# Performance work log

Hardware: AMD Instinct MI355X
Metric: run time of the kernel (lower is better)

## Reference

```python
import jax, jax.numpy as jnp
import numpy as np

B, T, C = 2, 2048, 2048
H = 16
HS = C // H           # 128
ROT = HS // 2         # 64 partial-rotary dims
BASE = 10000.0


def setup_inputs() -> dict:
    key = jax.random.key(0)
    ks = jax.random.split(key, 9)
    s = 1.0 / np.sqrt(C)
    return {
        "x": jax.random.normal(ks[0], (B, T, C), jnp.float32),
        "Wq": jax.random.normal(ks[1], (C, C), jnp.float32) * s,
        "bq": jax.random.normal(ks[2], (C,), jnp.float32) * 0.02,
        "Wk": jax.random.normal(ks[3], (C, C), jnp.float32) * s,
        "bk": jax.random.normal(ks[4], (C,), jnp.float32) * 0.02,
        "Wv": jax.random.normal(ks[5], (C, C), jnp.float32) * s,
        "bv": jax.random.normal(ks[6], (C,), jnp.float32) * 0.02,
        "Wo": jax.random.normal(ks[7], (C, C), jnp.float32) * s,
        "bo": jax.random.normal(ks[8], (C,), jnp.float32) * 0.02,
    }


def _rotate_half(u):
    u1, u2 = u[..., : u.shape[-1] // 2], u[..., u.shape[-1] // 2 :]
    return jnp.concatenate((-u2, u1), axis=-1)


def _rope_tables(t_len):
    inv_freq = 1.0 / (BASE ** (jnp.arange(0, ROT, 2, dtype=jnp.float32) / ROT))
    freqs = jnp.arange(t_len, dtype=jnp.float32)[:, None] * inv_freq[None, :]
    emb = jnp.concatenate((freqs, freqs), axis=-1)  # [T, ROT]
    return jnp.cos(emb), jnp.sin(emb)


def reference(x, Wq, bq, Wk, bk, Wv, bv, Wo, bo):
    Bs, Ts, Cs = x.shape
    q = (x @ Wq.T + bq).reshape(Bs, Ts, H, HS).transpose(0, 2, 1, 3)  # [B,H,T,HS]
    k = (x @ Wk.T + bk).reshape(Bs, Ts, H, HS).transpose(0, 2, 1, 3)
    v = (x @ Wv.T + bv).reshape(Bs, Ts, H, HS).transpose(0, 2, 1, 3)

    # partial rotary on first ROT dims of each head
    cos, sin = _rope_tables(Ts)  # [T, ROT] broadcast over B,H
    q_rot, q_pass = q[..., :ROT], q[..., ROT:]
    k_rot, k_pass = k[..., :ROT], k[..., ROT:]
    q_rot = q_rot * cos + _rotate_half(q_rot) * sin
    k_rot = k_rot * cos + _rotate_half(k_rot) * sin
    q = jnp.concatenate((q_rot, q_pass), axis=-1)
    k = jnp.concatenate((k_rot, k_pass), axis=-1)

    att = jnp.einsum("bhqd,bhkd->bhqk", q, k) * (1.0 / np.sqrt(HS))
    causal = jnp.tril(jnp.ones((Ts, Ts), dtype=bool))
    att = jnp.where(causal, att, jnp.float32(-jnp.inf))
    att = jax.nn.softmax(att, axis=-1)
    out = jnp.einsum("bhqk,bhkd->bhqd", att, v)          # [B,H,T,HS]
    out = out.transpose(0, 2, 1, 3).reshape(Bs, Ts, Cs)  # [B,T,C]
    return out @ Wo.T + bo
```

## Files before the change

### kernel.cpp

```cpp
#include <hip/hip_runtime.h>
#include <hip/hip_bf16.h>

#define Bdim 2
#define Tdim 2048
#define Cdim 2048
#define Hn   16

using bf16x8 = __attribute__((ext_vector_type(8))) short;
using f32x4  = __attribute__((ext_vector_type(4))) float;
using f32x16 = __attribute__((ext_vector_type(16))) float;
typedef __hip_bfloat16 bf16;

#define VMWAIT(n) asm volatile("s_waitcnt vmcnt(" #n ")" ::: "memory")
#define CROW(r, hi) (((r) & 3) + 8 * ((r) >> 2) + 4 * (hi))
#define QS2 ((float)(0.08838834764831845 * 1.4426950408889634))
#define THR2 11.5415603f

__device__ __forceinline__ void load_lds16(const void* g, void* l) {
  __builtin_amdgcn_global_load_lds(
      (const __attribute__((address_space(1))) void*)g,
      (__attribute__((address_space(3))) void*)l, 16, 0, 0);
}

__device__ __forceinline__ float bf2f(unsigned short u) {
  union { unsigned int i; float f; } x; x.i = ((unsigned int)u) << 16; return x.f;
}
__device__ __forceinline__ unsigned short f2bf(float f) {
  bf16 h = __float2bfloat16(f); return *(unsigned short*)&h;
}
__device__ __forceinline__ unsigned cvtpk(float lo, float hi) {
  unsigned r;
  asm volatile("v_cvt_pk_bf16_f32 %0, %1, %2" : "=v"(r) : "v"(lo), "v"(hi));
  return r;
}

__global__ __launch_bounds__(256) void cvt_all(const float* __restrict__ x,
                                               const float* __restrict__ w0,
                                               const float* __restrict__ w1,
                                               const float* __restrict__ w2,
                                               const float* __restrict__ w3,
                                               bf16* __restrict__ dx,
                                               bf16* __restrict__ d0,
                                               bf16* __restrict__ d1,
                                               bf16* __restrict__ d2,
                                               bf16* __restrict__ d3) {
  const int NX = (Bdim * Tdim * Cdim) / 4;
  const int NW = (Cdim * Cdim) / 4;
  int i = blockIdx.x * 256 + threadIdx.x;
  int stride = gridDim.x * 256;
  for (; i < NX + 4 * NW; i += stride) {
    const float* s; bf16* d; int j;
    if (i < NX) { s = x; d = dx; j = i; }
    else {
      int k = i - NX;
      int wsel = k >> 20;
      j = k & (NW - 1);
      s = wsel == 0 ? w0 : wsel == 1 ? w1 : wsel == 2 ? w2 : w3;
      d = wsel == 0 ? d0 : wsel == 1 ? d1 : wsel == 2 ? d2 : d3;
    }
    float4 v = ((const float4*)s)[j];
    ushort4 o;
    o.x = f2bf(v.x); o.y = f2bf(v.y); o.z = f2bf(v.z); o.w = f2bf(v.w);
    ((ushort4*)d)[j] = o;
  }
}

__global__ __launch_bounds__(256) void rope_tables_k(float2* __restrict__ cst) {
  int idx = blockIdx.x * blockDim.x + threadIdx.x;
  if (idx >= Tdim * 32) return;
  int t = idx >> 5, i = idx & 31;
  double f = pow(10000.0, -(double)i / 32.0);
  double ang = (double)t * f;
  cst[idx] = make_float2((float)cos(ang), (float)sin(ang));
}

__global__ __launch_bounds__(256, 2) void gemmQKV(
    const bf16* __restrict__ A, const bf16* __restrict__ Wcat,
    const float* __restrict__ b0, const float* __restrict__ b1, const float* __restrict__ b2,
    bf16* __restrict__ oq, bf16* __restrict__ ok, bf16* __restrict__ vt,
    const float2* __restrict__ cst) {
  extern __shared__ char lds[];
  const int tid = threadIdx.x, lane = tid & 63, wid = tid >> 6;
  const int l31 = lane & 31, hi = lane >> 5;
  const int wr = wid >> 1, wc = wid & 1;
  const int wbase = wid * 1024;

  const int q8 = gridDim.x >> 3;
  const int swz = ((int)blockIdx.x & 7) * q8 + ((int)blockIdx.x >> 3);
  const int bm = (swz >> 5) * 256;
  const int strip = swz & 31;

  const int rS = tid >> 2, sS = tid & 3;
  const int ssw = (sS ^ ((rS >> 1) & 3)) << 3;
  const bf16* thrA = A + (size_t)(bm + rS) * 2048 + ssw;
  const bf16* thrB = Wcat + (size_t)(strip * 192 + rS) * 2048 + ssw;

#define SA(T, DB) { load_lds16(thrA + (T) * 32, (DB) + wbase);                              \
                    load_lds16(thrA + (size_t)64 * 2048 + (T) * 32, (DB) + 4096 + wbase);   \
                    load_lds16(thrA + (size_t)128 * 2048 + (T) * 32, (DB) + 8192 + wbase);  \
                    load_lds16(thrA + (size_t)192 * 2048 + (T) * 32, (DB) + 12288 + wbase); }
#define SB(T, DB) { load_lds16(thrB + (T) * 32, (DB) + 16384 + wbase);                      \
                    load_lds16(thrB + (size_t)64 * 2048 + (T) * 32, (DB) + 20480 + wbase);  \
                    load_lds16(thrB + (size_t)128 * 2048 + (T) * 32, (DB) + 24576 + wbase); }

  f32x16 acc[4][3] = {};
  bf16x8 afr[4], bfr[3];
  const int q2 = (l31 >> 1) & 3;
  const int aoff = (wr * 128 + l31) * 64;
  const int boff = 16384 + (wc * 96 + l31) * 64;
  const int sl0 = (hi ^ q2) << 4;
  const int sl1 = sl0 ^ 32;

#define READF(PB, SL)                                                        \
  {                                                                          \
    const char* _p = (PB);                                                   \
    _Pragma("unroll")                                                        \
    for (int m_ = 0; m_ < 4; ++m_)                                           \
      afr[m_] = *(const bf16x8*)(_p + aoff + m_ * 2048 + (SL));              \
    _Pragma("unroll")                                                        \
    for (int n_ = 0; n_ < 3; ++n_)                                           \
      bfr[n_] = *(const bf16x8*)(_p + boff + n_ * 2048 + (SL));              \
  }

#define MF12()                                                               \
  __builtin_amdgcn_s_setprio(1);                                             \
  _Pragma("unroll")                                                          \
  for (int m_ = 0; m_ < 4; ++m_)                                             \
    _Pragma("unroll")                                                        \
    for (int n_ = 0; n_ < 3; ++n_)                                           \
      acc[m_][n_] = __builtin_amdgcn_mfma_f32_32x32x16_bf16(                 \
          afr[m_], bfr[n_], acc[m_][n_], 0, 0, 0);                           \
  __builtin_amdgcn_s_setprio(0);

  SA(0, lds); SB(0, lds);
  VMWAIT(0);
  __builtin_amdgcn_s_barrier();
  __builtin_amdgcn_sched_barrier(0);
  READF(lds, sl0);

  const int NT = 64;
  for (int t = 0; t < NT; ++t) {
    char* bufC = lds + (t & 1) * 28672;
    char* bufO = lds + ((t + 1) & 1) * 28672;
    if (t + 1 < NT) { SA(t + 1, bufO); SB(t + 1, bufO); }
    MF12();
    READF(bufC, sl1);
    MF12();
    if (t + 1 < NT) {
      VMWAIT(0);
      __builtin_amdgcn_s_barrier();
      __builtin_amdgcn_sched_barrier(0);
      READF(bufO, sl0);
    }
  }

  __syncthreads();
  if (wc == 1 && (strip & 1)) {
    const int col0 = strip * 192 + 96;
    const int mat = col0 >> 11;
    if (mat < 2) {
      const int oc0 = col0 & 2047;
      const float bv = (mat == 0 ? b0 : b1)[oc0 + l31];
      #pragma unroll
      for (int m = 0; m < 4; ++m)
        #pragma unroll
        for (int g = 0; g < 4; ++g) {
          f32x4 v;
          v[0] = acc[m][0][4 * g + 0] + bv;
          v[1] = acc[m][0][4 * g + 1] + bv;
          v[2] = acc[m][0][4 * g + 2] + bv;
          v[3] = acc[m][0][4 * g + 3] + bv;
          *(f32x4*)(lds + (((((wr * 4 + m) * 4 + g) * 2 + hi) * 32) + l31) * 16) = v;
        }
    }
  }
  __syncthreads();

  #pragma unroll
  for (int m = 0; m < 4; ++m) {
    const int rowb = bm + wr * 128 + m * 32;
    const int bb = rowb >> 11, tb = rowb & 2047;
    #pragma unroll
    for (int n = 0; n < 3; ++n) {
      const int col0 = strip * 192 + wc * 96 + n * 32;
      const int mat = col0 >> 11;
      const int oc0 = col0 & 2047;
      const float bv = (mat == 0 ? b0 : mat == 1 ? b1 : b2)[oc0 + l31];
      if (mat == 2) {
        const int hh = oc0 >> 7;
        bf16* dst = vt + ((size_t)((bb * 16 + hh) * 128 + (oc0 & 127) + l31)) * 2048 + tb;
        #pragma unroll
        for (int g = 0; g < 4; ++g) {
          ushort4 pk;
          pk.x = f2bf(acc[m][n][4 * g + 0] + bv);
          pk.y = f2bf(acc[m][n][4 * g + 1] + bv);
          pk.z = f2bf(acc[m][n][4 * g + 2] + bv);
          pk.w = f2bf(acc[m][n][4 * g + 3] + bv);
          *(ushort4*)(dst + g * 8 + hi * 4) = pk;
        }
      } else {
        const float qs = (mat == 0) ? QS2 : 1.0f;
        bf16* obf = (mat == 0) ? oq : ok;
        const float* bp = (mat == 0) ? b0 : b1;
        const int hb = (col0 >> 5) & 3;
        if (hb == 0) {
          if (n == 2) {
            #pragma unroll
            for (int g = 0; g < 4; ++g) {
              f32x4 ux = *(const f32x4*)(lds + (((((wr * 4 + m) * 4 + g) * 2 + hi) * 32) + l31) * 16);
              #pragma unroll
              for (int j = 0; j < 4; ++j) {
                const int r = 4 * g + j;
                const int row = rowb + j + 8 * g + 4 * hi;
                const int tt = row & 2047;
                float2 cs = cst[tt * 32 + l31];
                float u0 = acc[m][n][r] + bv;
                float u1 = ux[j];
                obf[(size_t)row * 2048 + oc0 + l31] =
                    __float2bfloat16((u0 * cs.x - u1 * cs.y) * qs);
                obf[(size_t)row * 2048 + oc0 + 32 + l31] =
                    __float2bfloat16((u1 * cs.x + u0 * cs.y) * qs);
              }
            }
          } else {
            const float bv1 = bp[oc0 + 32 + l31];
            #pragma unroll
            for (int r = 0; r < 16; ++r) {
              const int row = rowb + (r & 3) + 8 * (r >> 2) + 4 * hi;
              const int tt = row & 2047;
              float2 cs = cst[tt * 32 + l31];
              float u0 = acc[m][n][r] + bv;
              float u1 = acc[m][n + 1][r] + bv1;
              obf[(size_t)row * 2048 + oc0 + l31] =
                  __float2bfloat16((u0 * cs.x - u1 * cs.y) * qs);
              obf[(size_t)row * 2048 + oc0 + 32 + l31] =
                  __float2bfloat16((u1 * cs.x + u0 * cs.y) * qs);
            }
          }
        } else if (hb >= 2) {
          #pragma unroll
          for (int r = 0; r < 16; ++r) {
            const int row = rowb + (r & 3) + 8 * (r >> 2) + 4 * hi;
            obf[(size_t)row * 2048 + oc0 + l31] =
                __float2bfloat16((acc[m][n][r] + bv) * qs);
          }
        }
      }
    }
  }
#undef SA
#undef SB
#undef READF
#undef MF12
}

__global__ __launch_bounds__(512, 2) void gemmWo(
    const bf16* __restrict__ A, const bf16* __restrict__ W0,
    const float* __restrict__ b0, float* __restrict__ out, int K, int nby) {
  extern __shared__ char lds[];
  const int tid = threadIdx.x, lane = tid & 63, wid = tid >> 6;
  const int l15 = lane & 15, lhi = lane >> 4;
  const int wr = wid >> 2, wc = wid & 3;
  const int fb = (wc & 1) | ((wc >> 1) << 2);

  const int q8 = gridDim.x >> 3;
  const int swz = ((int)blockIdx.x & 7) * q8 + ((int)blockIdx.x >> 3);
  const int bm = (swz / nby) * 128, bn = (swz % nby) * 256;
  const bf16* Asrc = A + (size_t)bm * K;
  const bf16* Wsrc = W0 + (size_t)bn * K;

  const bf16 *sA0, *sA1, *sB00, *sB01, *sB10, *sB11;
  {
    int c = tid, r = c >> 3, sl = c & 7;
    size_t off = (size_t)r * K + ((sl ^ (r & 7)) << 3);
    sA0 = Asrc + off;
    sA1 = Asrc + (size_t)64 * K + off;
    sB00 = Wsrc + off;
    sB10 = Wsrc + (size_t)128 * K + off;
  }
  {
    int c = 512 + tid, r = c >> 3, sl = c & 7;
    size_t off = (size_t)r * K + ((sl ^ (r & 7)) << 3);
    sB01 = Wsrc + off;
    sB11 = Wsrc + (size_t)128 * K + off;
  }
  const int ldsA = wid * 1024;

#define SA0(t) load_lds16(sA0 + (t) * 64, lds + ((t) & 1) * 49152 + ldsA)
#define SA1(t) load_lds16(sA1 + (t) * 64, lds + ((t) & 1) * 49152 + 8192 + ldsA)
#define SB0(t) { load_lds16(sB00 + (t) * 64, lds + ((t) & 1) * 49152 + 16384 + ldsA); \
                 load_lds16(sB01 + (t) * 64, lds + ((t) & 1) * 49152 + 24576 + ldsA); }
#define SB1(t) { load_lds16(sB10 + (t) * 64, lds + ((t) & 1) * 49152 + 32768 + ldsA); \
                 load_lds16(sB11 + (t) * 64, lds + ((t) & 1) * 49152 + 40960 + ldsA); }

  f32x4 acc[4][4] = {};
  const int NT = K / 64;
  const int NI = NT / 2;
  const int asw = (l15 & 7) << 4;
  bf16x8 afr[2][2], bfr0[2][2], bfr1[2][2];

#define READ_A(BASE)                                                            \
  _Pragma("unroll")                                                             \
  for (int ii = 0; ii < 2; ++ii)                                                \
    _Pragma("unroll")                                                           \
    for (int kk = 0; kk < 2; ++kk)                                              \
      afr[ii][kk] = *(const bf16x8*)((BASE) + (wr * 32 + ii * 16 + l15) * 128   \
                                     + ((kk * 64 + lhi * 16) ^ asw));

#define READ_B(BASE, DST)                                                       \
  _Pragma("unroll")                                                             \
  for (int j = 0; j < 2; ++j)                                                   \
    _Pragma("unroll")                                                           \
    for (int kk = 0; kk < 2; ++kk)                                              \
      DST[j][kk] = *(const bf16x8*)((BASE) + ((fb + 2 * j) * 16 + l15) * 128    \
                                    + ((kk * 64 + lhi * 16) ^ asw));

#define MFMA_Q(MH, NH, BF)                                                      \
  __builtin_amdgcn_s_setprio(1);                                                \
  _Pragma("unroll")                                                             \
  for (int ii = 0; ii < 2; ++ii)                                                \
    _Pragma("unroll")                                                           \
    for (int j = 0; j < 2; ++j)                                                 \
      _Pragma("unroll")                                                         \
      for (int kk = 0; kk < 2; ++kk)                                            \
        acc[(MH) * 2 + ii][(NH) * 2 + j] =                                      \
            __builtin_amdgcn_mfma_f32_16x16x32_bf16(                            \
                afr[ii][kk], BF[j][kk], acc[(MH) * 2 + ii][(NH) * 2 + j], 0, 0, 0); \
  __builtin_amdgcn_s_setprio(0);

#define BAR_IN()                                                                \
  __builtin_amdgcn_s_barrier();                                                 \
  asm volatile("s_waitcnt lgkmcnt(0)" ::: "memory");                            \
  __builtin_amdgcn_sched_barrier(0);

#define BAR_OUT() __builtin_amdgcn_s_barrier();

  SA0(0); SB0(0); SB1(0); SA1(0);
  SA0(1); SB0(1); SB1(1);
  VMWAIT(5);
  __builtin_amdgcn_s_barrier();

  char* const buf0 = lds;
  char* const buf1 = lds + 49152;

  for (int i = 0; i < NI; ++i) {
    const int t0 = 2 * i, t1 = t0 + 1;
    const bool lastI = (i == NI - 1);

    READ_A(buf0);
    READ_B(buf0 + 16384, bfr0);
    SA1(t1);
    BAR_IN(); MFMA_Q(0, 0, bfr0); BAR_OUT();

    READ_B(buf0 + 32768, bfr1);
    if (!lastI) SA0(t0 + 2);
    BAR_IN(); MFMA_Q(0, 1, bfr1); BAR_OUT();

    READ_A(buf0 + 8192);
    if (!lastI) SB0(t0 + 2);
    BAR_IN(); MFMA_Q(1, 0, bfr0); BAR_OUT();

    if (!lastI) { SB1(t0 + 2); VMWAIT(5); } else VMWAIT(0);
    BAR_IN(); MFMA_Q(1, 1, bfr1); BAR_OUT();

    READ_A(buf1);
    READ_B(buf1 + 16384, bfr0);
    if (!lastI) SA1(t0 + 2);
    BAR_IN(); MFMA_Q(0, 0, bfr0); BAR_OUT();

    READ_B(buf1 + 32768, bfr1);
    if (!lastI) SA0(t1 + 2);
    BAR_IN(); MFMA_Q(0, 1, bfr1); BAR_OUT();

    READ_A(buf1 + 8192);
    if (!lastI) SB0(t1 + 2);
    BAR_IN(); MFMA_Q(1, 0, bfr0); BAR_OUT();

    if (!lastI) { SB1(t1 + 2); VMWAIT(5); }
    BAR_IN(); MFMA_Q(1, 1, bfr1); BAR_OUT();
  }

  #pragma unroll
  for (int mi = 0; mi < 4; ++mi) {
    const int row = bm + (mi >> 1) * 64 + wr * 32 + (mi & 1) * 16 + lhi * 4;
    #pragma unroll
    for (int nj = 0; nj < 4; ++nj) {
      const int col = bn + (nj >> 1) * 128 + (fb + 2 * (nj & 1)) * 16 + l15;
      const float bv = b0[col];
      #pragma unroll
      for (int r = 0; r < 4; ++r)
        out[(size_t)(row + r) * 2048 + col] = acc[mi][nj][r] + bv;
    }
  }
#undef SA0
#undef SA1
#undef SB0
#undef SB1
#undef READ_A
#undef READ_B
#undef MFMA_Q
#undef BAR_IN
#undef BAR_OUT
}

__global__ __launch_bounds__(256, 2) void attn_kernel(const bf16* __restrict__ Q,
                                                      const bf16* __restrict__ Kb,
                                                      const bf16* __restrict__ Vt,
                                                      bf16* __restrict__ O) {
  extern __shared__ char lds[];
  const int tid = threadIdx.x, lane = tid & 63, wave = tid >> 6;
  const int l31 = lane & 31, hi = lane >> 5;
  const int hi16 = hi << 4;

  const int bid = blockIdx.x;
  const int half = bid >> 8;
  const int idx = bid & 255;
  const int g = idx >> 5;
  const int qt = half ? g : (15 - g);
  const int bh = idx & 31;
  const int b = bh >> 4, h = bh & 15;
  const size_t bT = (size_t)b * Tdim;

  const int qb = qt * 128 + wave * 32;
  const int myq = qb + l31;

  bf16x8 qf[8];
  {
    const bf16* qrow = Q + (bT + myq) * Cdim + h * 128;
    #pragma unroll
    for (int ds = 0; ds < 8; ++ds)
      qf[ds] = *(const bf16x8*)(qrow + ds * 16 + hi * 8);
  }

  auto stageKV = [&](int kt) {
    const int k0 = kt * 64;
    char* kb = lds + (kt & 1) * 16384;
    char* vb = lds + 32768 + (kt & 1) * 16384;
    #pragma unroll
    for (int i = 0; i < 4; ++i) {
      int cb = i * 256 + wave * 64;
      int c = cb + lane;
      {
        int row = c >> 4, slot = c & 15;
        load_lds16(Kb + (bT + k0 + row) * Cdim + h * 128 + ((slot ^ (row & 7)) << 3),
                   kb + cb * 16);
      }
      {
        int row = c >> 3, slot = c & 7;
        load_lds16(Vt + ((size_t)(bh * 128 + row)) * Tdim + k0 + ((slot ^ (row & 7)) << 3),
                   vb + cb * 16);
      }
    }
  };

  f32x16 o[4] = {};
  float mrun = -1e30f, lrun = 0.f;

  const int nt = 2 * (qt + 1);
  stageKV(0);

  for (int kt = 0; kt < nt; ++kt) {
    if (kt + 1 < nt) { stageKV(kt + 1); VMWAIT(8); } else { VMWAIT(0); }
    __syncthreads();
    const char* kbuf = lds + (kt & 1) * 16384;
    const char* vbuf = lds + 32768 + (kt & 1) * 16384;
    const int k0 = kt * 64;

    const bool active = (k0 <= qb + 31);
    if (active) {
      f32x16 s0 = {}, s1 = {};
      const int krow0 = l31, krow1 = 32 + l31;
      const int ksw = (l31 & 7) << 4;
      __builtin_amdgcn_s_setprio(1);
      #pragma unroll
      for (int ds = 0; ds < 8; ++ds) {
        const int boff = (ds * 32 + hi16) ^ ksw;
        bf16x8 kf0 = *(const bf16x8*)(kbuf + krow0 * 256 + boff);
        bf16x8 kf1 = *(const bf16x8*)(kbuf + krow1 * 256 + boff);
        s0 = __builtin_amdgcn_mfma_f32_32x32x16_bf16(kf0, qf[ds], s0, 0, 0, 0);
        s1 = __builtin_amdgcn_mfma_f32_32x32x16_bf16(kf1, qf[ds], s1, 0, 0, 0);
      }
      __builtin_amdgcn_s_setprio(0);

      if (k0 + 63 > qb) {
        #pragma unroll
        for (int r = 0; r < 16; ++r) {
          const int key = k0 + CROW(r, hi);
          if (key > myq)      s0[r] = -1e30f;
          if (key + 32 > myq) s1[r] = -1e30f;
        }
      }

      float mx = s0[0];
      #pragma unroll
      for (int r = 1; r < 16; ++r) mx = fmaxf(mx, s0[r]);
      #pragma unroll
      for (int r = 0; r < 16; ++r) mx = fmaxf(mx, s1[r]);
      mx = fmaxf(mx, __shfl_xor(mx, 32));
      if (!__all(mx <= mrun + THR2)) {
        const float mnew = fmaxf(mrun, mx);
        const float scl = __builtin_amdgcn_exp2f(mrun - mnew);
        lrun *= scl;
        #pragma unroll
        for (int r = 0; r < 16; ++r) {
          const float sr = __shfl(scl, CROW(r, hi));
          o[0][r] *= sr; o[1][r] *= sr; o[2][r] *= sr; o[3][r] *= sr;
        }
        mrun = mnew;
      }
      float p0[16], p1[16];
      float ps = 0.f;
      #pragma unroll
      for (int r = 0; r < 16; ++r) {
        p0[r] = __builtin_amdgcn_exp2f(s0[r] - mrun); ps += p0[r];
        p1[r] = __builtin_amdgcn_exp2f(s1[r] - mrun); ps += p1[r];
      }
      ps += __shfl_xor(ps, 32);
      lrun += ps;

      unsigned u0[8], u1[8];
      #pragma unroll
      for (int gg = 0; gg < 4; ++gg) {
        u0[gg * 2 + 0] = cvtpk(p0[gg * 4 + 0], p0[gg * 4 + 1]);
        u0[gg * 2 + 1] = cvtpk(p0[gg * 4 + 2], p0[gg * 4 + 3]);
        u1[gg * 2 + 0] = cvtpk(p1[gg * 4 + 0], p1[gg * 4 + 1]);
        u1[gg * 2 + 1] = cvtpk(p1[gg * 4 + 2], p1[gg * 4 + 3]);
      }
      bf16x8 paf[4];
      #pragma unroll
      for (int s = 0; s < 2; ++s) {
        const unsigned* us = s ? u1 : u0;
        #pragma unroll
        for (int gp = 0; gp < 2; ++gp) {
          unsigned snd0 = hi ? us[4 * gp + 0] : us[4 * gp + 2];
          unsigned snd1 = hi ? us[4 * gp + 1] : us[4 * gp + 3];
          unsigned rcv0 = __shfl_xor((int)snd0, 32);
          unsigned rcv1 = __shfl_xor((int)snd1, 32);
          union { unsigned w[4]; bf16x8 v; } fr;
          if (hi == 0) {
            fr.w[0] = us[4 * gp + 0]; fr.w[1] = us[4 * gp + 1];
            fr.w[2] = rcv0;           fr.w[3] = rcv1;
          } else {
            fr.w[0] = rcv0;           fr.w[1] = rcv1;
            fr.w[2] = us[4 * gp + 2]; fr.w[3] = us[4 * gp + 3];
          }
          paf[s * 2 + gp] = fr.v;
        }
      }

      __builtin_amdgcn_s_setprio(1);
      #pragma unroll
      for (int dblk = 0; dblk < 4; ++dblk) {
        const int d = dblk * 32 + l31;
        const int vswz = (d & 7) << 4;
        #pragma unroll
        for (int ks = 0; ks < 4; ++ks) {
          bf16x8 vf = *(const bf16x8*)(vbuf + d * 128 + ((ks * 32 + hi16) ^ vswz));
          o[dblk] = __builtin_amdgcn_mfma_f32_32x32x16_bf16(paf[ks], vf, o[dblk], 0, 0, 0);
        }
      }
      __builtin_amdgcn_s_setprio(0);
    }
    __syncthreads();
  }

  const float inv = 1.f / lrun;
  #pragma unroll
  for (int r = 0; r < 16; ++r) {
    const float ir = __shfl(inv, CROW(r, hi));
    const int qrow = qb + CROW(r, hi);
    bf16* orow = O + (bT + qrow) * Cdim + h * 128;
    #pragma unroll
    for (int dblk = 0; dblk < 4; ++dblk)
      orow[dblk * 32 + l31] = __float2bfloat16(o[dblk][r] * ir);
  }
}

extern "C" void kernel_launch(void* const* d_in, const int* in_sizes, int n_in,
                              void* d_out, int out_size, void* d_ws, size_t ws_size,
                              hipStream_t stream) {
  const float* x  = (const float*)d_in[0];
  const float* Wq = (const float*)d_in[1];
  const float* bq = (const float*)d_in[2];
  const float* Wk = (const float*)d_in[3];
  const float* bk = (const float*)d_in[4];
  const float* Wv = (const float*)d_in[5];
  const float* bv = (const float*)d_in[6];
  const float* Wo = (const float*)d_in[7];
  const float* bo = (const float*)d_in[8];

  char* ws = (char*)d_ws;
  const size_t SZ_X  = (size_t)Bdim * Tdim * Cdim * 2;
  const size_t SZ_W  = (size_t)Cdim * Cdim * 2;
  bf16* x_bf  = (bf16*)(ws);
  bf16* Wq_bf = (bf16*)(ws + SZ_X);
  bf16* Wk_bf = (bf16*)(ws + SZ_X + SZ_W);
  bf16* Wv_bf = (bf16*)(ws + SZ_X + 2 * SZ_W);
  bf16* Wo_bf = (bf16*)(ws + SZ_X + 3 * SZ_W);
  bf16* q_bf  = (bf16*)(ws + SZ_X + 4 * SZ_W);
  bf16* k_bf  = (bf16*)(ws + 2 * SZ_X + 4 * SZ_W);
  bf16* v_t   = (bf16*)(ws + 3 * SZ_X + 4 * SZ_W);
  bf16* a_bf  = (bf16*)(ws + 4 * SZ_X + 4 * SZ_W);
  float2* cst = (float2*)(ws + 5 * SZ_X + 4 * SZ_W);

  const int K = Cdim;

  rope_tables_k<<<(Tdim * 32 + 255) / 256, 256, 0, stream>>>(cst);
  cvt_all<<<2048, 256, 0, stream>>>(x, Wq, Wk, Wv, Wo,
                                    x_bf, Wq_bf, Wk_bf, Wv_bf, Wo_bf);

  gemmQKV<<<512, 256, 57344, stream>>>(
      x_bf, Wq_bf, bq, bk, bv, q_bf, k_bf, v_t, cst);

  attn_kernel<<<512, 256, 65536, stream>>>(q_bf, k_bf, v_t, a_bf);

  gemmWo<<<256, 512, 98304, stream>>>(
      a_bf, Wo_bf, bo, (float*)d_out, K, 8);
}
```

Baseline: 236.2 us.

## Triple-buffer A tiles in QKV GEMM to prefetch two K-steps ahead

Result: no change. 236.2 us (-0.0%).

```diff
diff --git a/kernel.cpp b/kernel.cpp
--- a/kernel.cpp
+++ b/kernel.cpp
@@ -95,31 +95,32 @@
   const bf16* thrA = A + (size_t)(bm + rS) * 2048 + ssw;
   const bf16* thrB = Wcat + (size_t)(strip * 192 + rS) * 2048 + ssw;
 
-#define SA(T, DB) { load_lds16(thrA + (T) * 32, (DB) + wbase);                              \
-                    load_lds16(thrA + (size_t)64 * 2048 + (T) * 32, (DB) + 4096 + wbase);   \
-                    load_lds16(thrA + (size_t)128 * 2048 + (T) * 32, (DB) + 8192 + wbase);  \
-                    load_lds16(thrA + (size_t)192 * 2048 + (T) * 32, (DB) + 12288 + wbase); }
-#define SB(T, DB) { load_lds16(thrB + (T) * 32, (DB) + 16384 + wbase);                      \
-                    load_lds16(thrB + (size_t)64 * 2048 + (T) * 32, (DB) + 20480 + wbase);  \
-                    load_lds16(thrB + (size_t)128 * 2048 + (T) * 32, (DB) + 24576 + wbase); }
+#define SA(T, AB) { load_lds16(thrA + (T) * 32, (AB) + wbase);                              \
+                    load_lds16(thrA + (size_t)64 * 2048 + (T) * 32, (AB) + 4096 + wbase);   \
+                    load_lds16(thrA + (size_t)128 * 2048 + (T) * 32, (AB) + 8192 + wbase);  \
+                    load_lds16(thrA + (size_t)192 * 2048 + (T) * 32, (AB) + 12288 + wbase); }
+#define SB(T, BB) { load_lds16(thrB + (T) * 32, (BB) + wbase);                              \
+                    load_lds16(thrB + (size_t)64 * 2048 + (T) * 32, (BB) + 4096 + wbase);   \
+                    load_lds16(thrB + (size_t)128 * 2048 + (T) * 32, (BB) + 8192 + wbase); }
 
   f32x16 acc[4][3] = {};
   bf16x8 afr[4], bfr[3];
   const int q2 = (l31 >> 1) & 3;
   const int aoff = (wr * 128 + l31) * 64;
-  const int boff = 16384 + (wc * 96 + l31) * 64;
+  const int boff = (wc * 96 + l31) * 64;
   const int sl0 = (hi ^ q2) << 4;
   const int sl1 = sl0 ^ 32;
 
-#define READF(PB, SL)                                                        \
+#define READF(PA, PB, SL)                                                    \
   {                                                                          \
-    const char* _p = (PB);                                                   \
+    const char* _pa = (PA);                                                  \
+    const char* _pb = (PB);                                                  \
     _Pragma("unroll")                                                        \
     for (int m_ = 0; m_ < 4; ++m_)                                           \
-      afr[m_] = *(const bf16x8*)(_p + aoff + m_ * 2048 + (SL));              \
+      afr[m_] = *(const bf16x8*)(_pa + aoff + m_ * 2048 + (SL));             \
     _Pragma("unroll")                                                        \
     for (int n_ = 0; n_ < 3; ++n_)                                           \
-      bfr[n_] = *(const bf16x8*)(_p + boff + n_ * 2048 + (SL));              \
+      bfr[n_] = *(const bf16x8*)(_pb + boff + n_ * 2048 + (SL));             \
   }
 
 #define MF12()                                                               \
@@ -132,25 +133,38 @@
           afr[m_], bfr[n_], acc[m_][n_], 0, 0, 0);                           \
   __builtin_amdgcn_s_setprio(0);
 
-  SA(0, lds); SB(0, lds);
+  char* const A0 = lds;
+  char* const A1 = lds + 16384;
+  char* const A2 = lds + 32768;
+  char* const B0 = lds + 49152;
+  char* const B1 = lds + 61440;
+
+  SB(0, B0); SA(0, A0); SA(1, A1);
   VMWAIT(0);
   __builtin_amdgcn_s_barrier();
   __builtin_amdgcn_sched_barrier(0);
-  READF(lds, sl0);
-
+  READF(A0, B0, sl0);
+
+  char* pAc = A0;
+  char* pAn = A1;
+  char* pAs = A2;
   const int NT = 64;
+
   for (int t = 0; t < NT; ++t) {
-    char* bufC = lds + (t & 1) * 28672;
-    char* bufO = lds + ((t + 1) & 1) * 28672;
-    if (t + 1 < NT) { SA(t + 1, bufO); SB(t + 1, bufO); }
+    char* pBc = (t & 1) ? B1 : B0;
+    char* pBn = (t & 1) ? B0 : B1;
+    if (t + 1 < NT) SB(t + 1, pBn);
+    if (t + 2 < NT) SA(t + 2, pAs);
     MF12();
-    READF(bufC, sl1);
+    READF(pAc, pBc, sl1);
     MF12();
     if (t + 1 < NT) {
-      VMWAIT(0);
+      if (t + 2 < NT) { VMWAIT(4); }
+      else            { VMWAIT(0); }
       __builtin_amdgcn_s_barrier();
       __builtin_amdgcn_sched_barrier(0);
-      READF(bufO, sl0);
+      READF(pAn, pBn, sl0);
+      char* tmp = pAc; pAc = pAn; pAn = pAs; pAs = tmp;
     }
   }
 
@@ -609,7 +623,7 @@
   cvt_all<<<2048, 256, 0, stream>>>(x, Wq, Wk, Wv, Wo,
                                     x_bf, Wq_bf, Wk_bf, Wv_bf, Wo_bf);
 
-  gemmQKV<<<512, 256, 57344, stream>>>(
+  gemmQKV<<<512, 256, 73728, stream>>>(
       x_bf, Wq_bf, bq, bk, bv, q_bf, k_bf, v_t, cst);
 
   attn_kernel<<<512, 256, 65536, stream>>>(q_bf, k_bf, v_t, a_bf);
```
